# Optimization experiments

Measured on AMD Instinct MI355X. Metric: run time of the kernel, lower is better.

## Reference

```python
import jax, jax.numpy as jnp
import numpy as np

NQ = 8
NL = 3
DIM = 2 ** NQ


def _rx(psi, w, theta):
    # theta: scalar or [B]
    B = psi.shape[0]
    t = jnp.atleast_1d(theta).astype(jnp.float32)
    c = jnp.cos(t / 2)[:, None, None].astype(jnp.complex64)
    s = (-1j * jnp.sin(t / 2))[:, None, None].astype(jnp.complex64)
    p = psi.reshape(B, 2 ** w, 2, -1)
    s0, s1 = p[:, :, 0], p[:, :, 1]
    return jnp.stack([c * s0 + s * s1, s * s0 + c * s1], axis=2).reshape(B, DIM)


def _ry(psi, w, theta):
    B = psi.shape[0]
    t = jnp.atleast_1d(theta).astype(jnp.float32)
    c = jnp.cos(t / 2)[:, None, None].astype(jnp.complex64)
    s = jnp.sin(t / 2)[:, None, None].astype(jnp.complex64)
    p = psi.reshape(B, 2 ** w, 2, -1)
    s0, s1 = p[:, :, 0], p[:, :, 1]
    return jnp.stack([c * s0 - s * s1, s * s0 + c * s1], axis=2).reshape(B, DIM)


def _rz(psi, w, theta):
    B = psi.shape[0]
    t = jnp.atleast_1d(theta).astype(jnp.float32)
    e0 = jnp.exp(-0.5j * t.astype(jnp.complex64))[:, None, None]
    e1 = jnp.exp(0.5j * t.astype(jnp.complex64))[:, None, None]
    p = psi.reshape(B, 2 ** w, 2, -1)
    return jnp.stack([e0 * p[:, :, 0], e1 * p[:, :, 1]], axis=2).reshape(B, DIM)


def _cnot(psi, c, t):
    # control c, target t (wire 0 = most significant axis)
    B = psi.shape[0]
    a, b = (c, t) if c < t else (t, c)
    p = psi.reshape(B, 2 ** a, 2, 2 ** (b - a - 1), 2, -1)
    caxis = 2 if c < t else 4
    taxis = 4 if c < t else 2
    idx = [slice(None)] * 6
    idx[caxis] = 1
    sub = p[tuple(idx)]  # control=1 slab, caxis removed
    fl_axis = taxis - (1 if taxis > caxis else 0)
    p = p.at[tuple(idx)].set(jnp.flip(sub, axis=fl_axis))
    return p.reshape(B, DIM)


# PauliZ signs per wire: [NQ, 2^NQ]
_bits = (np.arange(DIM)[None, :] >> (NQ - 1 - np.arange(NQ)[:, None])) & 1
_Z_SIGNS = jnp.asarray((1 - 2 * _bits).astype(np.float32))


def _quantum_layer(enc, qrx, qry, qrz):
    # enc: [B, NQ] encoding angles; qrx/qry/qrz: [NL, NQ] scalar params
    B = enc.shape[0]
    psi = jnp.zeros((B, DIM), jnp.complex64).at[:, 0].set(1.0)
    for i in range(NQ):
        psi = _rx(psi, i, enc[:, i])
    for l in range(NL):
        for i in range(NQ):
            psi = _rx(psi, i, qrx[l, i])
            psi = _ry(psi, i, qry[l, i])
            psi = _rz(psi, i, qrz[l, i])
        for i in range(NQ - 1):
            psi = _cnot(psi, i, i + 1)
        psi = _cnot(psi, NQ - 1, 0)
    probs = psi.real ** 2 + psi.imag ** 2  # [B, 2^NQ]
    return probs @ _Z_SIGNS.T  # [B, NQ] <Z_i>


def _critic(x, w1, b1, w2, b2, qrx, qry, qrz, w3, b3, w4, b4):
    h = jax.nn.relu(x @ w1 + b1)
    enc = h @ w2 + b2
    ex = _quantum_layer(enc, qrx, qry, qrz)
    h2 = jax.nn.relu(ex @ w3 + b3)
    return h2 @ w4 + b4


def setup_inputs() -> dict:
    key = jax.random.key(0)
    ks = jax.random.split(key, 32)
    B, OBS, ACT, H = 65536, 96, 32, 256
    D = OBS + ACT

    def lin(k, fin, fout):
        return jax.random.normal(k, (fin, fout), jnp.float32) * (1.0 / np.sqrt(fin))

    inp = {
        'state': jax.random.normal(ks[0], (B, OBS), jnp.float32),
        'action': jax.random.normal(ks[1], (B, ACT), jnp.float32),
    }
    for ci, tag in enumerate(['a', 'b']):
        o = 2 + ci * 15
        inp['w1' + tag] = lin(ks[o + 0], D, H)
        inp['b1' + tag] = jnp.zeros((H,), jnp.float32)
        inp['w2' + tag] = lin(ks[o + 1], H, NQ)
        inp['b2' + tag] = jnp.zeros((NQ,), jnp.float32)
        inp['qrx' + tag] = jax.random.normal(ks[o + 2], (NL, NQ), jnp.float32)
        inp['qry' + tag] = jax.random.normal(ks[o + 3], (NL, NQ), jnp.float32)
        inp['qrz' + tag] = jax.random.normal(ks[o + 4], (NL, NQ), jnp.float32)
        inp['w3' + tag] = lin(ks[o + 5], NQ, H)
        inp['b3' + tag] = jnp.zeros((H,), jnp.float32)
        inp['w4' + tag] = lin(ks[o + 6], H, 1)
        inp['b4' + tag] = jnp.zeros((1,), jnp.float32)
    return inp


def reference(state, action,
              w1a, b1a, w2a, b2a, qrxa, qrya, qrza, w3a, b3a, w4a, b4a,
              w1b, b1b, w2b, b2b, qrxb, qryb, qrzb, w3b, b3b, w4b, b4b):
    x = jnp.concatenate([state, action], axis=1)
    q1 = _critic(x, w1a, b1a, w2a, b2a, qrxa, qrya, qrza, w3a, b3a, w4a, b4a)
    q2 = _critic(x, w1b, b1b, w2b, b2b, qrxb, qryb, qrzb, w3b, b3b, w4b, b4b)
    return (q1, q2)
```

## Files before the change

### kernel.cpp

```cpp
#include <hip/hip_runtime.h>
#include <math.h>


typedef __attribute__((ext_vector_type(8))) short bfrag_t;
typedef __attribute__((ext_vector_type(16))) float accv_t;

__device__ __forceinline__ unsigned short f2bf(float x) {
  unsigned u = __float_as_uint(x);
  u += 0x7FFFu + ((u >> 16) & 1u);
  return (unsigned short)(u >> 16);
}
__device__ __forceinline__ float bf2f(unsigned short h) {
  return __uint_as_float(((unsigned)h) << 16);
}
__device__ __forceinline__ unsigned pack2(float a, float b) {
  return (unsigned)f2bf(a) | ((unsigned)f2bf(b) << 16);
}

struct C2 { float r, i; };
__device__ __forceinline__ C2 cmul(C2 a, C2 b){ return C2{a.r*b.r - a.i*b.i, a.r*b.i + a.i*b.r}; }
__device__ __forceinline__ C2 cadd(C2 a, C2 b){ return C2{a.r+b.r, a.i+b.i}; }

#define APPLY2(A,Bx)                                                        \
  { float ar=re[A], ai=im[A], br=re[Bx], bi=im[Bx];                         \
    re[A]  = u00r*ar - u00i*ai + u01r*br - u01i*bi;                         \
    im[A]  = u00r*ai + u00i*ar + u01r*bi + u01i*br;                         \
    re[Bx] = u10r*ar - u10i*ai + u11r*br - u11i*bi;                         \
    im[Bx] = u10r*ai + u10i*ar + u11r*bi + u11i*br; }

__global__ __launch_bounds__(256)
void prep_weights(const float* __restrict__ qrxa, const float* __restrict__ qrya,
                  const float* __restrict__ qrza,
                  const float* __restrict__ qrxb, const float* __restrict__ qryb,
                  const float* __restrict__ qrzb,
                  const float* __restrict__ w1a, const float* __restrict__ w1b,
                  const float* __restrict__ w2a, const float* __restrict__ w2b,
                  const float* __restrict__ w3a, const float* __restrict__ w3b,
                  unsigned short* __restrict__ Bm, unsigned short* __restrict__ Gm,
                  unsigned short* __restrict__ w1p, unsigned short* __restrict__ w2p) {
  int blk = blockIdx.x;
  int tid = threadIdx.x;
  if (blk < 128) {
    __shared__ float sg[192];
    int c = blk >> 6;
    if (tid < 24) {
      const float* qx = c ? qrxb : qrxa;
      const float* qy = c ? qryb : qrya;
      const float* qz = c ? qrzb : qrza;
      int g = tid;
      float tx = 0.5f*qx[g], ty = 0.5f*qy[g], tz = 0.5f*qz[g];
      float cx = cosf(tx), sx = sinf(tx);
      float cy = cosf(ty), sy = sinf(ty);
      float cz = cosf(tz), sz = sinf(tz);
      C2 rx00{cx,0.f}, rx01{0.f,-sx}, rx10{0.f,-sx}, rx11{cx,0.f};
      C2 m00 = cadd(cmul(C2{cy,0.f},rx00), cmul(C2{-sy,0.f},rx10));
      C2 m01 = cadd(cmul(C2{cy,0.f},rx01), cmul(C2{-sy,0.f},rx11));
      C2 m10 = cadd(cmul(C2{sy,0.f},rx00), cmul(C2{cy,0.f},rx10));
      C2 m11 = cadd(cmul(C2{sy,0.f},rx01), cmul(C2{cy,0.f},rx11));
      C2 e0{cz,-sz}, e1{cz,sz};
      C2 u00 = cmul(e0,m00), u01 = cmul(e0,m01), u10 = cmul(e1,m10), u11 = cmul(e1,m11);
      float* o = sg + g*8;
      o[0]=u00.r; o[1]=u00.i; o[2]=u01.r; o[3]=u01.i;
      o[4]=u10.r; o[5]=u10.i; o[6]=u11.r; o[7]=u11.i;
    }
    __syncthreads();
    int lane = tid & 63;
    int wid = blk*4 + (tid >> 6);
    int bcol = wid & 255;
    int p = __popc(bcol) & 3;
    float phr = (p==0) ? 1.f : ((p==2) ? -1.f : 0.f);
    float phi = (p==1) ? -1.f : ((p==3) ? 1.f : 0.f);
    float re[4], im[4];
    #pragma unroll
    for (int j = 0; j < 4; ++j) {
      int idx = 4*lane + j;
      re[j] = (idx==bcol) ? phr : 0.f;
      im[j] = (idx==bcol) ? phi : 0.f;
    }
    #pragma unroll
    for (int l = 0; l < 3; ++l) {
      #pragma unroll
      for (int q = 0; q < 8; ++q) {
        const float* u = &sg[(size_t)(l*8 + q)*8];
        float u00r=u[0],u00i=u[1],u01r=u[2],u01i=u[3];
        float u10r=u[4],u10i=u[5],u11r=u[6],u11i=u[7];
        if (q < 6) {
          int m = 5-q, mask = 1<<m;
          bool s1 = ((lane >> m) & 1) != 0;
          float udr = s1?u11r:u00r, udi = s1?u11i:u00i;
          float uor = s1?u10r:u01r, uoi = s1?u10i:u01i;
          #pragma unroll
          for (int j = 0; j < 4; ++j) {
            float pr = __shfl_xor(re[j], mask);
            float pi = __shfl_xor(im[j], mask);
            float nr = udr*re[j] - udi*im[j] + uor*pr - uoi*pi;
            float ni = udr*im[j] + udi*re[j] + uor*pi + uoi*pr;
            re[j]=nr; im[j]=ni;
          }
        } else if (q == 6) { APPLY2(0,2); APPLY2(1,3); }
        else               { APPLY2(0,1); APPLY2(2,3); }
      }
      #pragma unroll
      for (int cq = 0; cq <= 4; ++cq) {
        int tmask = 1 << (4-cq);
        bool pred = ((lane >> (5-cq)) & 1) != 0;
        #pragma unroll
        for (int j = 0; j < 4; ++j) {
          float sr = __shfl_xor(re[j], tmask);
          float si = __shfl_xor(im[j], tmask);
          re[j] = pred ? sr : re[j];
          im[j] = pred ? si : im[j];
        }
      }
      { bool pred = (lane & 1) != 0;
        float t0, t1;
        t0 = pred?re[2]:re[0]; t1 = pred?re[0]:re[2]; re[0]=t0; re[2]=t1;
        t0 = pred?im[2]:im[0]; t1 = pred?im[0]:im[2]; im[0]=t0; im[2]=t1;
        t0 = pred?re[3]:re[1]; t1 = pred?re[1]:re[3]; re[1]=t0; re[3]=t1;
        t0 = pred?im[3]:im[1]; t1 = pred?im[1]:im[3]; im[1]=t0; im[3]=t1; }
      { float t;
        t=re[2]; re[2]=re[3]; re[3]=t;
        t=im[2]; im[2]=im[3]; im[3]=t; }
      { re[1]=__shfl_xor(re[1],32); im[1]=__shfl_xor(im[1],32);
        re[3]=__shfl_xor(re[3],32); im[3]=__shfl_xor(im[3],32); }
    }
    #pragma unroll
    for (int j = 0; j < 4; ++j) {
      int i = 4*lane + j;
      Bm[(size_t)(c*512 + i)*256 + bcol]       = f2bf(re[j]);
      Bm[(size_t)(c*512 + 256 + i)*256 + bcol] = f2bf(im[j]);
    }
  } else if (blk < 192) {
    int slot = (blk-128)*256 + tid;
    int n = slot & 255, h5 = (slot>>8)&1, ks = (slot>>9)&7, p = (slot>>12)&1, c = slot>>13;
    const float* w1c = c ? w1b : w1a;
    #pragma unroll
    for (int j = 0; j < 8; ++j) {
      float v = w1c[(size_t)(ks*16 + h5*8 + j)*256 + n];
      unsigned short hi = f2bf(v);
      w1p[(size_t)slot*8 + j] = p ? f2bf(v - bf2f(hi)) : hi;
    }
  } else if (blk < 200) {
    int slot = (blk-192)*256 + tid;
    int combo = slot >> 4, part = slot & 15;
    int h5 = combo&1, k16 = (combo>>1)&15, p = (combo>>5)&1, c = (combo>>6)&1;
    const float* w2c = c ? w2b : w2a;
    #pragma unroll
    for (int jj = 0; jj < 16; ++jj) {
      int idx = part*16 + jj;
      int il = idx >> 3, j = idx & 7;
      int n = k16*16 + h5*8 + j;
      float v = (il < 8) ? w2c[(size_t)n*8 + il] : 0.f;
      unsigned short hi = f2bf(v);
      w2p[(size_t)combo*256 + idx] = p ? f2bf(v - bf2f(hi)) : hi;
    }
  } else {
    int idx = (blk-200)*256 + tid;
    int c = idx >> 16, w = (idx >> 13) & 7, ks = (idx >> 9) & 15;
    int l = (idx >> 3) & 63, j = idx & 7;
    int n = 32*w + (l & 31);
    int i = ks*16 + (l >> 5)*8 + j;
    const float* w3 = c ? w3b : w3a;
    float s = 0.f;
    #pragma unroll
    for (int q = 0; q < 8; ++q) {
      float sg2 = ((i >> (7-q)) & 1) ? -1.f : 1.f;
      s += sg2 * w3[q*256 + n];
    }
    Gm[idx] = f2bf(s);
  }
}

__global__ __launch_bounds__(256, 2)
void enc_mfma(const float* __restrict__ state, const float* __restrict__ action,
              const unsigned short* __restrict__ w1p,
              const float* __restrict__ b1a, const float* __restrict__ b1b,
              const unsigned short* __restrict__ w2p,
              const float* __restrict__ b2a, const float* __restrict__ b2b,
              float* __restrict__ enc, int Bn) {
  __shared__ __align__(16) char Bx[2][16384];
  __shared__ __align__(16) float sb1[2][256];
  __shared__ float sb2[2][8];
  __shared__ __align__(16) float encw[4][2][32][8];
  int tid = threadIdx.x;
  int lane = tid & 63, w = tid >> 6, il = lane & 31, h5 = lane >> 5;
  int r0 = blockIdx.x * 64;

  sb1[0][tid] = b1a[tid];
  sb1[1][tid] = b1b[tid];
  if (tid < 8) { sb2[0][tid] = b2a[tid]; sb2[1][tid] = b2b[tid]; }

  {
    int m = tid >> 2, kq = tid & 3;
    const float4* st4 = (const float4*)state;
    const float4* ac4 = (const float4*)action;
    #pragma unroll
    for (int ks = 0; ks < 8; ++ks) {
      float4 v = (ks < 6) ? st4[(size_t)(r0+m)*24 + ks*4 + kq]
                          : ac4[(size_t)(r0+m)*8 + (ks-6)*4 + kq];
      unsigned short hx = f2bf(v.x), hy = f2bf(v.y), hz = f2bf(v.z), hw = f2bf(v.w);
      uint2 hh, ll;
      hh.x = (unsigned)hx | ((unsigned)hy << 16);
      hh.y = (unsigned)hz | ((unsigned)hw << 16);
      ll.x = (unsigned)f2bf(v.x - bf2f(hx)) | ((unsigned)f2bf(v.y - bf2f(hy)) << 16);
      ll.y = (unsigned)f2bf(v.z - bf2f(hz)) | ((unsigned)f2bf(v.w - bf2f(hw)) << 16);
      int off = ks*2048 + m*32 + kq*8;
      *(uint2*)(&Bx[0][off]) = hh;
      *(uint2*)(&Bx[1][off]) = ll;
    }
  }
  __syncthreads();

  for (int c = 0; c < 2; ++c) {
    accv_t A[2][2] = {{{},{}},{{},{}}};
    #pragma unroll
    for (int ks = 0; ks < 8; ++ks) {
      bfrag_t a0h, a0l, a1h, a1l;
      {
        size_t b0 = ((size_t)((c*2+0)*8 + ks)*2 + h5)*256;
        size_t b1 = ((size_t)((c*2+1)*8 + ks)*2 + h5)*256;
        int t0 = 2*w, t1 = 2*w+1;
        a0h = *(const bfrag_t*)(w1p + (b0 + t0*32 + il)*8);
        a0l = *(const bfrag_t*)(w1p + (b1 + t0*32 + il)*8);
        a1h = *(const bfrag_t*)(w1p + (b0 + t1*32 + il)*8);
        a1l = *(const bfrag_t*)(w1p + (b1 + t1*32 + il)*8);
      }
      bfrag_t b0h = *(const bfrag_t*)(&Bx[0][ks*2048 + il*32 + h5*16]);
      bfrag_t b0l = *(const bfrag_t*)(&Bx[1][ks*2048 + il*32 + h5*16]);
      bfrag_t b1h_ = *(const bfrag_t*)(&Bx[0][ks*2048 + (32+il)*32 + h5*16]);
      bfrag_t b1l_ = *(const bfrag_t*)(&Bx[1][ks*2048 + (32+il)*32 + h5*16]);
      A[0][0] = __builtin_amdgcn_mfma_f32_32x32x16_bf16(a0h, b0h, A[0][0], 0,0,0);
      A[0][0] = __builtin_amdgcn_mfma_f32_32x32x16_bf16(a0h, b0l, A[0][0], 0,0,0);
      A[0][0] = __builtin_amdgcn_mfma_f32_32x32x16_bf16(a0l, b0h, A[0][0], 0,0,0);
      A[0][1] = __builtin_amdgcn_mfma_f32_32x32x16_bf16(a0h, b1h_, A[0][1], 0,0,0);
      A[0][1] = __builtin_amdgcn_mfma_f32_32x32x16_bf16(a0h, b1l_, A[0][1], 0,0,0);
      A[0][1] = __builtin_amdgcn_mfma_f32_32x32x16_bf16(a0l, b1h_, A[0][1], 0,0,0);
      A[1][0] = __builtin_amdgcn_mfma_f32_32x32x16_bf16(a1h, b0h, A[1][0], 0,0,0);
      A[1][0] = __builtin_amdgcn_mfma_f32_32x32x16_bf16(a1h, b0l, A[1][0], 0,0,0);
      A[1][0] = __builtin_amdgcn_mfma_f32_32x32x16_bf16(a1l, b0h, A[1][0], 0,0,0);
      A[1][1] = __builtin_amdgcn_mfma_f32_32x32x16_bf16(a1h, b1h_, A[1][1], 0,0,0);
      A[1][1] = __builtin_amdgcn_mfma_f32_32x32x16_bf16(a1h, b1l_, A[1][1], 0,0,0);
      A[1][1] = __builtin_amdgcn_mfma_f32_32x32x16_bf16(a1l, b1h_, A[1][1], 0,0,0);
    }
    #pragma unroll
    for (int nt = 0; nt < 2; ++nt) {
      #pragma unroll
      for (int g = 0; g < 4; ++g) {
        float4 bb = *(const float4*)&sb1[c][(2*w+nt)*32 + 8*g + 4*h5];
        float bba[4] = {bb.x, bb.y, bb.z, bb.w};
        #pragma unroll
        for (int jj = 0; jj < 4; ++jj) {
          A[nt][0][4*g+jj] = fmaxf(A[nt][0][4*g+jj] + bba[jj], 0.f);
          A[nt][1][4*g+jj] = fmaxf(A[nt][1][4*g+jj] + bba[jj], 0.f);
        }
      }
    }
    accv_t Cm[2] = {{},{}};
    #pragma unroll
    for (int k2 = 0; k2 < 4; ++k2) {
      int k16 = 4*w + k2;
      bfrag_t g2h = *(const bfrag_t*)(w2p + ((size_t)((c*2+0)*16 + k16)*2 + h5)*256 + il*8);
      bfrag_t g2l = *(const bfrag_t*)(w2p + ((size_t)((c*2+1)*16 + k16)*2 + h5)*256 + il*8);
      #pragma unroll
      for (int mt = 0; mt < 2; ++mt) {
        unsigned ph[2][2], pl[2][2];
        #pragma unroll
        for (int gi = 0; gi < 2; ++gi) {
          int G = 2*k2 + gi, nt = G >> 2, g = G & 3;
          float f0 = A[nt][mt][4*g+0], f1 = A[nt][mt][4*g+1];
          float f2 = A[nt][mt][4*g+2], f3 = A[nt][mt][4*g+3];
          unsigned short h0 = f2bf(f0), h1 = f2bf(f1), h2 = f2bf(f2), h3 = f2bf(f3);
          ph[gi][0] = (unsigned)h0 | ((unsigned)h1 << 16);
          ph[gi][1] = (unsigned)h2 | ((unsigned)h3 << 16);
          pl[gi][0] = (unsigned)f2bf(f0 - bf2f(h0)) | ((unsigned)f2bf(f1 - bf2f(h1)) << 16);
          pl[gi][1] = (unsigned)f2bf(f2 - bf2f(h2)) | ((unsigned)f2bf(f3 - bf2f(h3)) << 16);
        }
        union { bfrag_t v; unsigned u[4]; } FH, FL;
        #pragma unroll
        for (int r = 0; r < 2; ++r) {
          unsigned own_h = h5 ? ph[1][r] : ph[0][r];
          unsigned alt_h = h5 ? ph[0][r] : ph[1][r];
          unsigned rec_h = __shfl_xor((int)alt_h, 32);
          FH.u[r]   = h5 ? rec_h : own_h;
          FH.u[2+r] = h5 ? own_h : rec_h;
          unsigned own_l = h5 ? pl[1][r] : pl[0][r];
          unsigned alt_l = h5 ? pl[0][r] : pl[1][r];
          unsigned rec_l = __shfl_xor((int)alt_l, 32);
          FL.u[r]   = h5 ? rec_l : own_l;
          FL.u[2+r] = h5 ? own_l : rec_l;
        }
        Cm[mt] = __builtin_amdgcn_mfma_f32_32x32x16_bf16(g2h, FH.v, Cm[mt], 0,0,0);
        Cm[mt] = __builtin_amdgcn_mfma_f32_32x32x16_bf16(g2h, FL.v, Cm[mt], 0,0,0);
        Cm[mt] = __builtin_amdgcn_mfma_f32_32x32x16_bf16(g2l, FH.v, Cm[mt], 0,0,0);
      }
    }
    *(float4*)&encw[w][0][il][4*h5] = make_float4(Cm[0][0], Cm[0][1], Cm[0][2], Cm[0][3]);
    *(float4*)&encw[w][1][il][4*h5] = make_float4(Cm[1][0], Cm[1][1], Cm[1][2], Cm[1][3]);
    __syncthreads();
    #pragma unroll
    for (int half = 0; half < 2; ++half) {
      int s = tid + half*256;
      int e = s & 7, mm = s >> 3;
      float v = sb2[c][e];
      #pragma unroll
      for (int ww = 0; ww < 4; ++ww) v += encw[ww][mm>>5][mm&31][e];
      enc[((size_t)c*Bn + r0 + mm)*8 + e] = v;
    }
    __syncthreads();
  }
}

__device__ __forceinline__ void a_build(float4 ea, float4 eb, char* Ab, int ag2, int am) {
  float c0,s0,c1,s1,c2,s2,c3,s3,c4,s4,c5,s5,c6,s6,c7,s7;
  __sincosf(0.5f*ea.x, &s0, &c0);
  __sincosf(0.5f*ea.y, &s1, &c1);
  __sincosf(0.5f*ea.z, &s2, &c2);
  __sincosf(0.5f*ea.w, &s3, &c3);
  __sincosf(0.5f*eb.x, &s4, &c4);
  __sincosf(0.5f*eb.y, &s5, &c5);
  __sincosf(0.5f*eb.z, &s6, &c6);
  __sincosf(0.5f*eb.w, &s7, &c7);
  float v0 = (ag2&8) ? s0 : c0;
  float v1 = (ag2&4) ? s1 : c1;
  float v2 = (ag2&2) ? s2 : c2;
  float v3 = (ag2&1) ? s3 : c3;
  float top = v0*v1*v2*v3;
  float hA = top*c4, hB = top*s4;
  float p67[4];
  p67[0] = c6*c7; p67[1] = c6*s7; p67[2] = s6*c7; p67[3] = s6*s7;
  float low[8];
  #pragma unroll
  for (int j = 0; j < 8; ++j) low[j] = ((j&4) ? s5 : c5) * p67[j&3];
  union { bfrag_t v; unsigned u[4]; } pk;
  #pragma unroll
  for (int k = 0; k < 4; ++k) pk.u[k] = pack2(hA*low[2*k], hA*low[2*k+1]);
  *(bfrag_t*)(Ab + ag2*1024 + am*16) = pk.v;
  #pragma unroll
  for (int k = 0; k < 4; ++k) pk.u[k] = pack2(hB*low[2*k], hB*low[2*k+1]);
  *(bfrag_t*)(Ab + ag2*1024 + 512 + am*16) = pk.v;
}

__global__ __launch_bounds__(512, 2)
void qgemm(const float* __restrict__ enc,
           const unsigned short* __restrict__ Bm, const unsigned short* __restrict__ Gm,
           const float* __restrict__ b3a, const float* __restrict__ w4a, const float* __restrict__ b4a,
           const float* __restrict__ b3b, const float* __restrict__ w4b, const float* __restrict__ b4b,
           float* __restrict__ out, int Bn) {
  __shared__ __align__(16) char APq[132096];
  char* A0 = APq;
  char* A1 = APq + 16384;
  char* P0 = APq + 32768;
  char* P1 = APq + 49664;
  float* qtmp = (float*)(APq + 66560);

  int tid = threadIdx.x;
  int lane = tid & 63;
  int w = tid >> 6;
  int il = lane & 31;
  int h5 = lane >> 5;

  int c = blockIdx.x >> 7;
  int rowblock = blockIdx.x & 127;
  int rowsPerBlock = Bn >> 7;
  int npairs = rowsPerBlock >> 6;

  bfrag_t bf0[16], bf1[16];
  {
    const unsigned short* base = Bm + ((size_t)(c*512 + 32*w + il)*256 + h5*8);
    #pragma unroll
    for (int ks = 0; ks < 16; ++ks) {
      bf0[ks] = *(const bfrag_t*)(base + ks*16);
      bf1[ks] = *(const bfrag_t*)(base + 256*256 + ks*16);
    }
  }
  int n2 = 32*w + il;
  const float* b3c = c ? b3b : b3a;
  const float* w4c = c ? w4b : w4a;
  const float* b4c = c ? b4b : b4a;
  float b3v = b3c[n2];
  float w4v = w4c[n2];
  float b4v = b4c[0];
  const unsigned short* Gbase = Gm + ((size_t)(c*8 + w)*16)*512 + lane*8;
  int pwbase = (n2>>4)*1056 + ((n2>>3)&1)*512 + (n2&7)*2;
  int rowAdd = 4*h5;

  int am = tid & 31, ag2 = tid >> 5;
  const float* encb = enc + ((size_t)c*Bn)*8;
  int rbase = rowblock*rowsPerBlock;

  {
    const float* ep0 = encb + (size_t)(rbase + am)*8;
    float4 pa0 = *(const float4*)ep0, pb0 = *(const float4*)(ep0 + 4);
    const float* ep1 = encb + (size_t)(rbase + 32 + am)*8;
    float4 pa1 = *(const float4*)ep1, pb1 = *(const float4*)(ep1 + 4);
    a_build(pa0, pb0, A0, ag2, am);
    a_build(pa1, pb1, A1, ag2, am);
  }
  __syncthreads();

  for (int st2 = 0; st2 < npairs; ++st2) {
    int r0 = rbase + st2*64;
    {
      accv_t acc0 = {}, acc1 = {};
      #pragma unroll
      for (int ks = 0; ks < 16; ++ks) {
        bfrag_t af = *(const bfrag_t*)(A0 + ks*1024 + lane*16);
        acc0 = __builtin_amdgcn_mfma_f32_32x32x16_bf16(af, bf0[ks], acc0, 0, 0, 0);
        acc1 = __builtin_amdgcn_mfma_f32_32x32x16_bf16(af, bf1[ks], acc1, 0, 0, 0);
      }
      #pragma unroll
      for (int r = 0; r < 16; ++r) {
        float P = acc0[r]*acc0[r] + acc1[r]*acc1[r];
        int row = (r&3) + 8*(r>>2) + rowAdd;
        *(unsigned short*)(P0 + pwbase + row*16) = f2bf(P);
      }
    }
    {
      accv_t acc0 = {}, acc1 = {};
      #pragma unroll
      for (int ks = 0; ks < 16; ++ks) {
        bfrag_t af = *(const bfrag_t*)(A1 + ks*1024 + lane*16);
        acc0 = __builtin_amdgcn_mfma_f32_32x32x16_bf16(af, bf0[ks], acc0, 0, 0, 0);
        acc1 = __builtin_amdgcn_mfma_f32_32x32x16_bf16(af, bf1[ks], acc1, 0, 0, 0);
      }
      #pragma unroll
      for (int r = 0; r < 16; ++r) {
        float P = acc0[r]*acc0[r] + acc1[r]*acc1[r];
        int row = (r&3) + 8*(r>>2) + rowAdd;
        *(unsigned short*)(P1 + pwbase + row*16) = f2bf(P);
      }
    }
    __syncthreads();
    float4 na0, nb0, na1, nb1;
    bool more = (st2 + 1 < npairs);
    if (more) {
      const float* ep0 = encb + (size_t)(r0 + 64 + am)*8;
      na0 = *(const float4*)ep0; nb0 = *(const float4*)(ep0 + 4);
      const float* ep1 = encb + (size_t)(r0 + 96 + am)*8;
      na1 = *(const float4*)ep1; nb1 = *(const float4*)(ep1 + 4);
    }
    accv_t acc2a = {}, acc2b = {};
    #pragma unroll 4
    for (int ks = 0; ks < 16; ++ks) {
      bfrag_t gf  = *(const bfrag_t*)(Gbase + ks*512);
      bfrag_t pf0 = *(const bfrag_t*)(P0 + ks*1056 + lane*16);
      bfrag_t pf1 = *(const bfrag_t*)(P1 + ks*1056 + lane*16);
      acc2a = __builtin_amdgcn_mfma_f32_32x32x16_bf16(pf0, gf, acc2a, 0, 0, 0);
      acc2b = __builtin_amdgcn_mfma_f32_32x32x16_bf16(pf1, gf, acc2b, 0, 0, 0);
    }
    #pragma unroll
    for (int r = 0; r < 16; ++r) {
      int row = (r&3) + 8*(r>>2) + rowAdd;
      qtmp[row*256 + n2]        = fmaxf(acc2a[r] + b3v, 0.f) * w4v;
      qtmp[(32 + row)*256 + n2] = fmaxf(acc2b[r] + b3v, 0.f) * w4v;
    }
    if (more) {
      a_build(na0, nb0, A0, ag2, am);
      a_build(na1, nb1, A1, ag2, am);
    }
    __syncthreads();
    {
      int row = tid >> 3, seg = tid & 7;
      const float* qrow = qtmp + row*256;
      float s = 0.f;
      #pragma unroll
      for (int t = 0; t < 8; ++t) {
        float4 a = *(const float4*)(qrow + t*32 + seg*4);
        s += (a.x + a.y) + (a.z + a.w);
      }
      s += __shfl_xor(s, 1);
      s += __shfl_xor(s, 2);
      s += __shfl_xor(s, 4);
      if (seg == 0) out[(size_t)c*Bn + r0 + row] = s + b4v;
    }
  }
}

extern "C" void kernel_launch(void* const* d_in, const int* in_sizes, int n_in,
                              void* d_out, int out_size, void* d_ws, size_t ws_size,
                              hipStream_t stream) {
  (void)n_in; (void)out_size; (void)ws_size;
  const float* state  = (const float*)d_in[0];
  const float* action = (const float*)d_in[1];
  const float* w1a=(const float*)d_in[2];  const float* b1a=(const float*)d_in[3];
  const float* w2a=(const float*)d_in[4];  const float* b2a=(const float*)d_in[5];
  const float* qrxa=(const float*)d_in[6]; const float* qrya=(const float*)d_in[7];
  const float* qrza=(const float*)d_in[8];
  const float* w3a=(const float*)d_in[9];  const float* b3a=(const float*)d_in[10];
  const float* w4a=(const float*)d_in[11]; const float* b4a=(const float*)d_in[12];
  const float* w1b=(const float*)d_in[13]; const float* b1b=(const float*)d_in[14];
  const float* w2b=(const float*)d_in[15]; const float* b2b=(const float*)d_in[16];
  const float* qrxb=(const float*)d_in[17];const float* qryb=(const float*)d_in[18];
  const float* qrzb=(const float*)d_in[19];
  const float* w3b=(const float*)d_in[20]; const float* b3b=(const float*)d_in[21];
  const float* w4b=(const float*)d_in[22]; const float* b4b=(const float*)d_in[23];

  int B = in_sizes[0] / 96;
  char* wsb = (char*)d_ws;
  unsigned short* Bmat = (unsigned short*)(wsb);
  unsigned short* Gmat = (unsigned short*)(wsb + 524288);
  unsigned short* w1p  = (unsigned short*)(wsb + 786432);
  unsigned short* w2p  = (unsigned short*)(wsb + 1048576);
  float* enc           = (float*)(wsb + 1114112);

  prep_weights<<<712, 256, 0, stream>>>(qrxa,qrya,qrza,qrxb,qryb,qrzb,
                                        w1a,w1b,w2a,w2b,w3a,w3b,
                                        Bmat,Gmat,w1p,w2p);
  enc_mfma<<<B/64, 256, 0, stream>>>(state,action,w1p,b1a,b1b,w2p,b2a,b2b,enc,B);
  qgemm<<<256, 512, 0, stream>>>(enc, Bmat, Gmat, b3a, w4a, b4a, b3b, w4b, b4b,
                                 (float*)d_out, B);
}
```

Baseline: 217.5 us.

## Halve enc_mfma rows per block to 32 and raise occupancy bound

```diff
diff --git a/kernel.cpp b/kernel.cpp
--- a/kernel.cpp
+++ b/kernel.cpp
@@ -171,31 +171,33 @@
   }
 }
 
-__global__ __launch_bounds__(256, 2)
+__global__ __launch_bounds__(256, 4)
 void enc_mfma(const float* __restrict__ state, const float* __restrict__ action,
               const unsigned short* __restrict__ w1p,
               const float* __restrict__ b1a, const float* __restrict__ b1b,
               const unsigned short* __restrict__ w2p,
               const float* __restrict__ b2a, const float* __restrict__ b2b,
               float* __restrict__ enc, int Bn) {
-  __shared__ __align__(16) char Bx[2][16384];
+  __shared__ __align__(16) char Bx[2][8192];
   __shared__ __align__(16) float sb1[2][256];
   __shared__ float sb2[2][8];
-  __shared__ __align__(16) float encw[4][2][32][8];
+  __shared__ __align__(16) float encw[4][32][8];
   int tid = threadIdx.x;
   int lane = tid & 63, w = tid >> 6, il = lane & 31, h5 = lane >> 5;
-  int r0 = blockIdx.x * 64;
+  int r0 = blockIdx.x * 32;
 
   sb1[0][tid] = b1a[tid];
   sb1[1][tid] = b1b[tid];
   if (tid < 8) { sb2[0][tid] = b2a[tid]; sb2[1][tid] = b2b[tid]; }
 
   {
-    int m = tid >> 2, kq = tid & 3;
+    int m = tid >> 3, q8 = tid & 7;
     const float4* st4 = (const float4*)state;
     const float4* ac4 = (const float4*)action;
     #pragma unroll
-    for (int ks = 0; ks < 8; ++ks) {
+    for (int j = 0; j < 4; ++j) {
+      int f = j*8 + q8;
+      int ks = f >> 2, kq = f & 3;
       float4 v = (ks < 6) ? st4[(size_t)(r0+m)*24 + ks*4 + kq]
                           : ac4[(size_t)(r0+m)*8 + (ks-6)*4 + kq];
       unsigned short hx = f2bf(v.x), hy = f2bf(v.y), hz = f2bf(v.z), hw = f2bf(v.w);
@@ -204,7 +206,7 @@
       hh.y = (unsigned)hz | ((unsigned)hw << 16);
       ll.x = (unsigned)f2bf(v.x - bf2f(hx)) | ((unsigned)f2bf(v.y - bf2f(hy)) << 16);
       ll.y = (unsigned)f2bf(v.z - bf2f(hz)) | ((unsigned)f2bf(v.w - bf2f(hw)) << 16);
-      int off = ks*2048 + m*32 + kq*8;
+      int off = ks*1024 + m*32 + kq*8;
       *(uint2*)(&Bx[0][off]) = hh;
       *(uint2*)(&Bx[1][off]) = ll;
     }
@@ -212,7 +214,7 @@
   __syncthreads();
 
   for (int c = 0; c < 2; ++c) {
-    accv_t A[2][2] = {{{},{}},{{},{}}};
+    accv_t A[2] = {{},{}};
     #pragma unroll
     for (int ks = 0; ks < 8; ++ks) {
       bfrag_t a0h, a0l, a1h, a1l;
@@ -225,22 +227,14 @@
         a1h = *(const bfrag_t*)(w1p + (b0 + t1*32 + il)*8);
         a1l = *(const bfrag_t*)(w1p + (b1 + t1*32 + il)*8);
       }
-      bfrag_t b0h = *(const bfrag_t*)(&Bx[0][ks*2048 + il*32 + h5*16]);
-      bfrag_t b0l = *(const bfrag_t*)(&Bx[1][ks*2048 + il*32 + h5*16]);
-      bfrag_t b1h_ = *(const bfrag_t*)(&Bx[0][ks*2048 + (32+il)*32 + h5*16]);
-      bfrag_t b1l_ = *(const bfrag_t*)(&Bx[1][ks*2048 + (32+il)*32 + h5*16]);
-      A[0][0] = __builtin_amdgcn_mfma_f32_32x32x16_bf16(a0h, b0h, A[0][0], 0,0,0);
-      A[0][0] = __builtin_amdgcn_mfma_f32_32x32x16_bf16(a0h, b0l, A[0][0], 0,0,0);
-      A[0][0] = __builtin_amdgcn_mfma_f32_32x32x16_bf16(a0l, b0h, A[0][0], 0,0,0);
-      A[0][1] = __builtin_amdgcn_mfma_f32_32x32x16_bf16(a0h, b1h_, A[0][1], 0,0,0);
-      A[0][1] = __builtin_amdgcn_mfma_f32_32x32x16_bf16(a0h, b1l_, A[0][1], 0,0,0);
-      A[0][1] = __builtin_amdgcn_mfma_f32_32x32x16_bf16(a0l, b1h_, A[0][1], 0,0,0);
-      A[1][0] = __builtin_amdgcn_mfma_f32_32x32x16_bf16(a1h, b0h, A[1][0], 0,0,0);
-      A[1][0] = __builtin_amdgcn_mfma_f32_32x32x16_bf16(a1h, b0l, A[1][0], 0,0,0);
-      A[1][0] = __builtin_amdgcn_mfma_f32_32x32x16_bf16(a1l, b0h, A[1][0], 0,0,0);
-      A[1][1] = __builtin_amdgcn_mfma_f32_32x32x16_bf16(a1h, b1h_, A[1][1], 0,0,0);
-      A[1][1] = __builtin_amdgcn_mfma_f32_32x32x16_bf16(a1h, b1l_, A[1][1], 0,0,0);
-      A[1][1] = __builtin_amdgcn_mfma_f32_32x32x16_bf16(a1l, b1h_, A[1][1], 0,0,0);
+      bfrag_t b0h = *(const bfrag_t*)(&Bx[0][ks*1024 + il*32 + h5*16]);
+      bfrag_t b0l = *(const bfrag_t*)(&Bx[1][ks*1024 + il*32 + h5*16]);
+      A[0] = __builtin_amdgcn_mfma_f32_32x32x16_bf16(a0h, b0h, A[0], 0,0,0);
+      A[0] = __builtin_amdgcn_mfma_f32_32x32x16_bf16(a0h, b0l, A[0], 0,0,0);
+      A[0] = __builtin_amdgcn_mfma_f32_32x32x16_bf16(a0l, b0h, A[0], 0,0,0);
+      A[1] = __builtin_amdgcn_mfma_f32_32x32x16_bf16(a1h, b0h, A[1], 0,0,0);
+      A[1] = __builtin_amdgcn_mfma_f32_32x32x16_bf16(a1h, b0l, A[1], 0,0,0);
+      A[1] = __builtin_amdgcn_mfma_f32_32x32x16_bf16(a1l, b0h, A[1], 0,0,0);
     }
     #pragma unroll
     for (int nt = 0; nt < 2; ++nt) {
@@ -250,60 +244,53 @@
         float bba[4] = {bb.x, bb.y, bb.z, bb.w};
         #pragma unroll
         for (int jj = 0; jj < 4; ++jj) {
-          A[nt][0][4*g+jj] = fmaxf(A[nt][0][4*g+jj] + bba[jj], 0.f);
-          A[nt][1][4*g+jj] = fmaxf(A[nt][1][4*g+jj] + bba[jj], 0.f);
+          A[nt][4*g+jj] = fmaxf(A[nt][4*g+jj] + bba[jj], 0.f);
         }
       }
     }
-    accv_t Cm[2] = {{},{}};
+    accv_t Cm = {};
     #pragma unroll
     for (int k2 = 0; k2 < 4; ++k2) {
       int k16 = 4*w + k2;
       bfrag_t g2h = *(const bfrag_t*)(w2p + ((size_t)((c*2+0)*16 + k16)*2 + h5)*256 + il*8);
       bfrag_t g2l = *(const bfrag_t*)(w2p + ((size_t)((c*2+1)*16 + k16)*2 + h5)*256 + il*8);
-      #pragma unroll
-      for (int mt = 0; mt < 2; ++mt) {
-        unsigned ph[2][2], pl[2][2];
-        #pragma unroll
-        for (int gi = 0; gi < 2; ++gi) {
-          int G = 2*k2 + gi, nt = G >> 2, g = G & 3;
-          float f0 = A[nt][mt][4*g+0], f1 = A[nt][mt][4*g+1];
-          float f2 = A[nt][mt][4*g+2], f3 = A[nt][mt][4*g+3];
-          unsigned short h0 = f2bf(f0), h1 = f2bf(f1), h2 = f2bf(f2), h3 = f2bf(f3);
-          ph[gi][0] = (unsigned)h0 | ((unsigned)h1 << 16);
-          ph[gi][1] = (unsigned)h2 | ((unsigned)h3 << 16);
-          pl[gi][0] = (unsigned)f2bf(f0 - bf2f(h0)) | ((unsigned)f2bf(f1 - bf2f(h1)) << 16);
-          pl[gi][1] = (unsigned)f2bf(f2 - bf2f(h2)) | ((unsigned)f2bf(f3 - bf2f(h3)) << 16);
-        }
-        union { bfrag_t v; unsigned u[4]; } FH, FL;
-        #pragma unroll
-        for (int r = 0; r < 2; ++r) {
-          unsigned own_h = h5 ? ph[1][r] : ph[0][r];
-          unsigned alt_h = h5 ? ph[0][r] : ph[1][r];
-          unsigned rec_h = __shfl_xor((int)alt_h, 32);
-          FH.u[r]   = h5 ? rec_h : own_h;
-          FH.u[2+r] = h5 ? own_h : rec_h;
-          unsigned own_l = h5 ? pl[1][r] : pl[0][r];
-          unsigned alt_l = h5 ? pl[0][r] : pl[1][r];
-          unsigned rec_l = __shfl_xor((int)alt_l, 32);
-          FL.u[r]   = h5 ? rec_l : own_l;
-          FL.u[2+r] = h5 ? own_l : rec_l;
-        }
-        Cm[mt] = __builtin_amdgcn_mfma_f32_32x32x16_bf16(g2h, FH.v, Cm[mt], 0,0,0);
-        Cm[mt] = __builtin_amdgcn_mfma_f32_32x32x16_bf16(g2h, FL.v, Cm[mt], 0,0,0);
-        Cm[mt] = __builtin_amdgcn_mfma_f32_32x32x16_bf16(g2l, FH.v, Cm[mt], 0,0,0);
-      }
-    }
-    *(float4*)&encw[w][0][il][4*h5] = make_float4(Cm[0][0], Cm[0][1], Cm[0][2], Cm[0][3]);
-    *(float4*)&encw[w][1][il][4*h5] = make_float4(Cm[1][0], Cm[1][1], Cm[1][2], Cm[1][3]);
+      unsigned ph[2][2], pl[2][2];
+      #pragma unroll
+      for (int gi = 0; gi < 2; ++gi) {
+        int G = 2*k2 + gi, nt = G >> 2, g = G & 3;
+        float f0 = A[nt][4*g+0], f1 = A[nt][4*g+1];
+        float f2 = A[nt][4*g+2], f3 = A[nt][4*g+3];
+        unsigned short h0 = f2bf(f0), h1 = f2bf(f1), h2 = f2bf(f2), h3 = f2bf(f3);
+        ph[gi][0] = (unsigned)h0 | ((unsigned)h1 << 16);
+        ph[gi][1] = (unsigned)h2 | ((unsigned)h3 << 16);
+        pl[gi][0] = (unsigned)f2bf(f0 - bf2f(h0)) | ((unsigned)f2bf(f1 - bf2f(h1)) << 16);
+        pl[gi][1] = (unsigned)f2bf(f2 - bf2f(h2)) | ((unsigned)f2bf(f3 - bf2f(h3)) << 16);
+      }
+      union { bfrag_t v; unsigned u[4]; } FH, FL;
+      #pragma unroll
+      for (int r = 0; r < 2; ++r) {
+        unsigned own_h = h5 ? ph[1][r] : ph[0][r];
+        unsigned alt_h = h5 ? ph[0][r] : ph[1][r];
+        unsigned rec_h = __shfl_xor((int)alt_h, 32);
+        FH.u[r]   = h5 ? rec_h : own_h;
+        FH.u[2+r] = h5 ? own_h : rec_h;
+        unsigned own_l = h5 ? pl[1][r] : pl[0][r];
+        unsigned alt_l = h5 ? pl[0][r] : pl[1][r];
+        unsigned rec_l = __shfl_xor((int)alt_l, 32);
+        FL.u[r]   = h5 ? rec_l : own_l;
+        FL.u[2+r] = h5 ? own_l : rec_l;
+      }
+      Cm = __builtin_amdgcn_mfma_f32_32x32x16_bf16(g2h, FH.v, Cm, 0,0,0);
+      Cm = __builtin_amdgcn_mfma_f32_32x32x16_bf16(g2h, FL.v, Cm, 0,0,0);
+      Cm = __builtin_amdgcn_mfma_f32_32x32x16_bf16(g2l, FH.v, Cm, 0,0,0);
+    }
+    *(float4*)&encw[w][il][4*h5] = make_float4(Cm[0], Cm[1], Cm[2], Cm[3]);
     __syncthreads();
-    #pragma unroll
-    for (int half = 0; half < 2; ++half) {
-      int s = tid + half*256;
-      int e = s & 7, mm = s >> 3;
+    {
+      int e = tid & 7, mm = tid >> 3;
       float v = sb2[c][e];
       #pragma unroll
-      for (int ww = 0; ww < 4; ++ww) v += encw[ww][mm>>5][mm&31][e];
+      for (int ww = 0; ww < 4; ++ww) v += encw[ww][mm][e];
       enc[((size_t)c*Bn + r0 + mm)*8 + e] = v;
     }
     __syncthreads();
@@ -506,7 +493,7 @@
   prep_weights<<<712, 256, 0, stream>>>(qrxa,qrya,qrza,qrxb,qryb,qrzb,
                                         w1a,w1b,w2a,w2b,w3a,w3b,
                                         Bmat,Gmat,w1p,w2p);
-  enc_mfma<<<B/64, 256, 0, stream>>>(state,action,w1p,b1a,b1b,w2p,b2a,b2b,enc,B);
+  enc_mfma<<<B/32, 256, 0, stream>>>(state,action,w1p,b1a,b1b,w2p,b2a,b2b,enc,B);
   qgemm<<<256, 512, 0, stream>>>(enc, Bmat, Gmat, b3a, w4a, b4a, b3b, w4b, b4b,
                                  (float*)d_out, B);
 }
```

New measurement: 223.8 us. 2.9% more time.
